# Performance work log

Measured on AMD Instinct MI355X. Metric: run time of the kernel, lower is better.

The kernel has to match this reference:

```python
import jax, jax.numpy as jnp
import numpy as np

EPS = 1e-5
THRESH = 1.5


def _compute_one(x, g_w, g_b, phi_w, phi_b, W_w, W_b, gamma, beta):
    # x: (c, w, h, z) -- single sample (torch code calls compute_x with batch 1)
    c, w, h, z = x.shape
    nz = z // 2
    # AdaptiveAvgPool3d(1) on x.permute(0,4,2,3,1): mean over (w, h, c) per z-slice -> (z,)
    p = x.mean(axis=(0, 1, 2))
    xp = x * p[None, None, None, :]
    # 1x1x1 conv projections (note: self.theta is defined but unused in the original)
    g_x = jnp.einsum('ic,cwhz->iwhz', g_w, x) + g_b[:, None, None, None]
    phi_x = jnp.einsum('ic,cwhz->iwhz', phi_w, xp) + phi_b[:, None, None, None]
    # MaxPool3d kernel (1,1,2): non-overlapping max pairs along z
    g_x = g_x.reshape(-1, w, h, nz, 2).max(axis=-1)      # (ic, w, h, nz)
    phi_x = phi_x.reshape(-1, w, h, nz, 2).max(axis=-1)  # (ic, w, h, nz)
    # theta_x: (x*p).permute(0,2,3,4,1).view(w*h, z, c)
    theta = xp.transpose(1, 2, 3, 0).reshape(w * h, z, c)
    # phi: permute(0,2,3,1,4).view(w*h, ic, nz)
    phi_m = phi_x.transpose(1, 2, 0, 3).reshape(w * h, -1, nz)
    # g: permute(0,2,3,4,1).view(w*h, nz, ic)
    g_m = g_x.transpose(1, 2, 3, 0).reshape(w * h, nz, -1)
    f = jnp.einsum('bzc,bcn->bzn', theta, phi_m)          # (wh, z, nz)
    a = jax.nn.softmax(f, axis=-1)
    y = jnp.einsum('bzn,bni->bzi', a, g_m)                # (wh, z, ic)
    y = y.reshape(w, h, z, -1).transpose(3, 0, 1, 2)      # (ic, w, h, z)
    wy = jnp.einsum('ci,iwhz->cwhz', W_w, y) + W_b[:, None, None, None]
    # BatchNorm3d in training mode on a single-sample batch: per-channel stats over (w,h,z)
    mu = wy.mean(axis=(1, 2, 3), keepdims=True)
    var = wy.var(axis=(1, 2, 3), keepdims=True)
    wy = (wy - mu) * jax.lax.rsqrt(var + EPS)
    wy = wy * gamma[:, None, None, None] + beta[:, None, None, None]
    return wy + x


def setup_inputs() -> dict:
    key = jax.random.key(0)
    ks = jax.random.split(key, 10)
    b, c, w, h, z = 2, 64, 64, 64, 64
    ic = c  # inter_channels defaults to in_channels
    x = jax.random.normal(ks[0], (b, c, w, h, z), dtype=jnp.float32)
    # spacings in [0, 3): some samples fall above spacing_thresh=1.5 (identity branch)
    spacings = jax.random.uniform(ks[1], (b, 3), dtype=jnp.float32) * 3.0
    g_w = jax.random.normal(ks[2], (ic, c), dtype=jnp.float32) * 0.1
    g_b = jax.random.normal(ks[3], (ic,), dtype=jnp.float32) * 0.1
    phi_w = jax.random.normal(ks[4], (ic, c), dtype=jnp.float32) * 0.1
    phi_b = jax.random.normal(ks[5], (ic,), dtype=jnp.float32) * 0.1
    W_w = jax.random.normal(ks[6], (c, ic), dtype=jnp.float32) * 0.1
    W_b = jax.random.normal(ks[7], (c,), dtype=jnp.float32) * 0.1
    gamma = jax.random.normal(ks[8], (c,), dtype=jnp.float32) * 0.1
    beta = jax.random.normal(ks[9], (c,), dtype=jnp.float32) * 0.1
    return {"x": x, "spacings": spacings, "g_w": g_w, "g_b": g_b,
            "phi_w": phi_w, "phi_b": phi_b, "W_w": W_w, "W_b": W_b,
            "gamma": gamma, "beta": beta}


def reference(x, spacings, g_w, g_b, phi_w, phi_b, W_w, W_b, gamma, beta):
    out = jax.vmap(_compute_one, in_axes=(0,) + (None,) * 8)(
        x, g_w, g_b, phi_w, phi_b, W_w, W_b, gamma, beta)
    use = (spacings[:, -1] <= THRESH)[:, None, None, None, None]
    return jnp.where(use, out, x)
```

## Files before the change

### kernel.cpp

```cpp
#include <hip/hip_runtime.h>
#include <hip/hip_bf16.h>
#include <math.h>

#define THRESH_SP 1.5f
#define WHZc   262144
#define CWHZc  16777216

#define WS_PSUM   0
#define WS_SLOT   128
#define WS_ZERO_N 8320
#define WS_W16_BYTE  65536
#define WS_WY_BYTE   131072
#define WS_W16_NEED  (WS_W16_BYTE + 3u*4096u*2u)
#define WS_WY_NEED   (WS_WY_BYTE + 2u*CWHZc*2u)

typedef __attribute__((ext_vector_type(8))) short bf16x8;
typedef __attribute__((ext_vector_type(4))) float floatx4;

#define MFMA(a, b, c) __builtin_amdgcn_mfma_f32_16x16x32_bf16((a), (b), (c), 0, 0, 0)

__device__ __forceinline__ unsigned short f2b(float f) {
    __hip_bfloat16 h = __float2bfloat16(f);
    return __builtin_bit_cast(unsigned short, h);
}
__device__ __forceinline__ float b2f(unsigned short h) {
    unsigned int u = ((unsigned int)h) << 16;
    return __builtin_bit_cast(float, u);
}
__device__ __forceinline__ bf16x8 ldfrag(const unsigned short* p, int elem_off) {
    return *(const bf16x8*)(p + elem_off);
}

__global__ __launch_bounds__(256) void k_prep(const float* __restrict__ gw,
                                              const float* __restrict__ pw,
                                              const float* __restrict__ Ww,
                                              float* __restrict__ ws,
                                              unsigned short* __restrict__ w16,
                                              int usew16) {
    const int i = blockIdx.x * 256 + threadIdx.x;
    if (i < WS_ZERO_N) ws[i] = 0.0f;
    if (usew16 && i < 4096) {
        w16[i]        = f2b(gw[i]);
        w16[4096 + i] = f2b(pw[i]);
        w16[8192 + i] = f2b(Ww[i]);
    }
}

__global__ __launch_bounds__(256) void k_pmean(const float* __restrict__ x,
                                               const float* __restrict__ sp,
                                               float* __restrict__ ws) {
    const int b = blockIdx.x >> 9;
    if (sp[b*3 + 2] > THRESH_SP) return;
    const int jb = blockIdx.x & 511;
    __shared__ float s[64];
    const int t = threadIdx.x;
    if (t < 64) s[t] = 0.0f;
    __syncthreads();
    const int idx4 = jb * 256 + t;
    const int z0 = (idx4 & 15) * 4;
    float a0 = 0.f, a1 = 0.f, a2 = 0.f, a3 = 0.f;
    const float* xb = x + (size_t)b * CWHZc;
#pragma unroll 4
    for (int it = 0; it < 32; ++it) {
        const float4 v = *(const float4*)&xb[(size_t)(idx4 + it * 131072) * 4];
        a0 += v.x; a1 += v.y; a2 += v.z; a3 += v.w;
    }
    a0 += __shfl_xor(a0, 16); a0 += __shfl_xor(a0, 32);
    a1 += __shfl_xor(a1, 16); a1 += __shfl_xor(a1, 32);
    a2 += __shfl_xor(a2, 16); a2 += __shfl_xor(a2, 32);
    a3 += __shfl_xor(a3, 16); a3 += __shfl_xor(a3, 32);
    if ((t & 63) < 16) {
        unsafeAtomicAdd(&s[z0 + 0], a0);
        unsafeAtomicAdd(&s[z0 + 1], a1);
        unsafeAtomicAdd(&s[z0 + 2], a2);
        unsafeAtomicAdd(&s[z0 + 3], a3);
    }
    __syncthreads();
    if (t < 64) unsafeAtomicAdd(&ws[WS_PSUM + b * 64 + t], s[t]);
}

#define L_WG     0
#define L_WP     9216
#define L_XA     18432
#define L_GPA    27648
#define L_PHA    32768
#define L_XB     37376
#define L_GPB    46592
#define L_PHB    51712
#define L_ATB    56320
#define L_BIAS   61440
#define L_PS     62208
#define L_TOTAL  62464

__global__ __launch_bounds__(512, 4) void k_main(
    const float* __restrict__ x, const float* __restrict__ sp,
    const float* __restrict__ gw, const float* __restrict__ gb,
    const float* __restrict__ pw, const float* __restrict__ pb,
    const float* __restrict__ Wwp, const float* __restrict__ Wbp,
    float* __restrict__ out, unsigned short* __restrict__ wy16, int use16,
    const unsigned short* __restrict__ w16, int usew16,
    float* __restrict__ ws) {
    const int blk = blockIdx.x;
    const int b = blk >> 11;
    if (sp[b*3 + 2] > THRESH_SP) return;
    const int whpair = (blk & 2047) * 2;

    __shared__ char smem[L_TOTAL];
    unsigned short* wg   = (unsigned short*)(smem + L_WG);
    unsigned short* wp   = (unsigned short*)(smem + L_WP);
    float*          bias = (float*)(smem + L_BIAS);
    float*          p_s  = (float*)(smem + L_PS);
    float*          statsf = (float*)(smem + L_PHA);

    const int t   = threadIdx.x;
    const int wv  = t >> 6;
    const int cid = wv >> 2;
    const int tt  = t & 255;
    const int l   = t & 63;
    const int lr  = l & 15;
    const int lq  = l >> 4;
    const int zt  = (wv & 3) << 4;

    unsigned short* xT   = (unsigned short*)(smem + (cid ? L_XB  : L_XA));
    unsigned short* gpT  = (unsigned short*)(smem + (cid ? L_GPB : L_GPA));
    unsigned short* phpN = (unsigned short*)(smem + (cid ? L_PHB : L_PHA));
    unsigned short* aT   = (unsigned short*)(smem + (cid ? L_ATB : L_WG));

    const int wh    = whpair + cid;
    const int xbase = b * CWHZc + wh * 64;

#pragma unroll
    for (int k = 0; k < 4; ++k) {
        const int f = tt + (k << 8);
        const int c = f & 63, zq = f >> 6;
        const float4 v = *(const float4*)&x[xbase + c * WHZc + zq * 4];
        xT[(zq*4 + 0)*72 + c] = f2b(v.x);
        xT[(zq*4 + 1)*72 + c] = f2b(v.y);
        xT[(zq*4 + 2)*72 + c] = f2b(v.z);
        xT[(zq*4 + 3)*72 + c] = f2b(v.w);
    }
    if (usew16) {
#pragma unroll
        for (int k = 0; k < 2; ++k) {
            const int f = t + (k << 9);
            const int mat = f >> 9;
            const int i = (f & 511) >> 3, seg = f & 7;
            unsigned short* dst = mat ? wp : wg;
            *(uint4*)&dst[i*72 + seg*8] = *(const uint4*)&w16[mat*4096 + i*64 + seg*8];
        }
    } else {
#pragma unroll
        for (int k = 0; k < 4; ++k) {
            const int f = t + (k << 9);
            const int mat = f >> 10, ff = f & 1023;
            const int i = ff >> 4, c4 = ff & 15;
            const float* src = mat ? pw : gw;
            unsigned short* dst = mat ? wp : wg;
            const float4 v = *(const float4*)&src[i*64 + c4*4];
            uint2 pk;
            pk.x = (unsigned)f2b(v.x) | ((unsigned)f2b(v.y) << 16);
            pk.y = (unsigned)f2b(v.z) | ((unsigned)f2b(v.w) << 16);
            *(uint2*)&dst[i*72 + c4*4] = pk;
        }
    }
    if (t < 192) bias[t] = (t < 64) ? gb[t] : (t < 128) ? pb[t - 64] : Wbp[t - 128];
    if (t < 64)  p_s[t] = ws[WS_PSUM + b*64 + t] * (1.0f / 262144.0f);
    __syncthreads();

    const bf16x8 a0 = ldfrag(xT, (zt + lr)*72 + lq*8);
    const bf16x8 a1 = ldfrag(xT, (zt + lr)*72 + lq*8 + 32);
    const float pz0 = p_s[zt + lq*4 + 0], pz1 = p_s[zt + lq*4 + 1];
    const float pz2 = p_s[zt + lq*4 + 2], pz3 = p_s[zt + lq*4 + 3];

    {
        const int n0 = (zt >> 1) + lq*2;
#pragma unroll
        for (int ti = 0; ti < 4; ++ti) {
            const int i = ti*16 + lr;
            const float bv = bias[i];
            floatx4 acc = {bv, bv, bv, bv};
            acc = MFMA(a0, ldfrag(wg, i*72 + lq*8), acc);
            acc = MFMA(a1, ldfrag(wg, i*72 + lq*8 + 32), acc);
            unsigned int pk = (unsigned)f2b(fmaxf(acc[0], acc[1])) |
                              ((unsigned)f2b(fmaxf(acc[2], acc[3])) << 16);
            *(unsigned int*)&gpT[i*40 + n0] = pk;
        }
    }
    __syncthreads();

    {
        const int n0 = (zt >> 1) + lq*2;
#pragma unroll
        for (int ti = 0; ti < 4; ++ti) {
            const int i = ti*16 + lr;
            floatx4 acc = {0.f, 0.f, 0.f, 0.f};
            acc = MFMA(a0, ldfrag(wp, i*72 + lq*8), acc);
            acc = MFMA(a1, ldfrag(wp, i*72 + lq*8 + 32), acc);
            const float bv = bias[64 + i];
            const float v0 = fmaf(acc[0], pz0, bv), v1 = fmaf(acc[1], pz1, bv);
            const float v2 = fmaf(acc[2], pz2, bv), v3 = fmaf(acc[3], pz3, bv);
            phpN[n0*72 + i]       = f2b(fmaxf(v0, v1));
            phpN[(n0 + 1)*72 + i] = f2b(fmaxf(v2, v3));
        }
    }
    __syncthreads();

    {
        floatx4 f0 = {0.f, 0.f, 0.f, 0.f}, f1 = {0.f, 0.f, 0.f, 0.f};
        f0 = MFMA(a0, ldfrag(phpN, lr*72 + lq*8), f0);
        f0 = MFMA(a1, ldfrag(phpN, lr*72 + lq*8 + 32), f0);
        f1 = MFMA(a0, ldfrag(phpN, (16 + lr)*72 + lq*8), f1);
        f1 = MFMA(a1, ldfrag(phpN, (16 + lr)*72 + lq*8 + 32), f1);
        if (usew16) {
            const int i = t >> 3, seg = t & 7;
            *(uint4*)&wp[i*72 + seg*8] = *(const uint4*)&w16[8192 + i*64 + seg*8];
        } else {
#pragma unroll
            for (int k = 0; k < 2; ++k) {
                const int f = t + (k << 9);
                const int i = f >> 4, c4 = f & 15;
                const float4 v = *(const float4*)&Wwp[i*64 + c4*4];
                uint2 pk;
                pk.x = (unsigned)f2b(v.x) | ((unsigned)f2b(v.y) << 16);
                pk.y = (unsigned)f2b(v.z) | ((unsigned)f2b(v.w) << 16);
                *(uint2*)&wp[i*72 + c4*4] = pk;
            }
        }
        const float pz[4] = {pz0, pz1, pz2, pz3};
#pragma unroll
        for (int r = 0; r < 4; ++r) {
            const float fr0 = f0[r] * pz[r], fr1 = f1[r] * pz[r];
            float m = fmaxf(fr0, fr1);
            m = fmaxf(m, __shfl_xor(m, 1)); m = fmaxf(m, __shfl_xor(m, 2));
            m = fmaxf(m, __shfl_xor(m, 4)); m = fmaxf(m, __shfl_xor(m, 8));
            const float e0 = __expf(fr0 - m), e1 = __expf(fr1 - m);
            float s = e0 + e1;
            s += __shfl_xor(s, 1); s += __shfl_xor(s, 2);
            s += __shfl_xor(s, 4); s += __shfl_xor(s, 8);
            const float inv = 1.0f / s;
            const int z = zt + lq*4 + r;
            aT[z*40 + lr]      = f2b(e0 * inv);
            aT[z*40 + lr + 16] = f2b(e1 * inv);
        }
    }
    __syncthreads();

    {
        if (t < 128) statsf[t] = 0.0f;
        const bf16x8 av = ldfrag(aT, (zt + lr)*40 + lq*8);
#pragma unroll
        for (int ti = 0; ti < 4; ++ti) {
            floatx4 acc = {0.f, 0.f, 0.f, 0.f};
            acc = MFMA(av, ldfrag(gpT, (ti*16 + lr)*40 + lq*8), acc);
#pragma unroll
            for (int r = 0; r < 4; ++r)
                xT[(zt + lq*4 + r)*72 + ti*16 + lr] = f2b(acc[r]);
        }
    }
    __syncthreads();

    {
        const bf16x8 y0 = ldfrag(xT, (zt + lr)*72 + lq*8);
        const bf16x8 y1 = ldfrag(xT, (zt + lr)*72 + lq*8 + 32);
#pragma unroll
        for (int ti = 0; ti < 4; ++ti) {
            const int co = ti*16 + lr;
            const float bv = bias[128 + co];
            floatx4 acc = {bv, bv, bv, bv};
            acc = MFMA(y0, ldfrag(wp, co*72 + lq*8), acc);
            acc = MFMA(y1, ldfrag(wp, co*72 + lq*8 + 32), acc);
            if (use16) {
                uint2 pk;
                pk.x = (unsigned)f2b(acc[0]) | ((unsigned)f2b(acc[1]) << 16);
                pk.y = (unsigned)f2b(acc[2]) | ((unsigned)f2b(acc[3]) << 16);
                *(uint2*)&wy16[(size_t)xbase + co * WHZc + zt + lq*4] = pk;
            } else {
                *(float4*)&out[xbase + co * WHZc + zt + lq*4] = *(float4*)&acc;
            }
            float s1 = acc[0] + acc[1] + acc[2] + acc[3];
            float s2 = acc[0]*acc[0] + acc[1]*acc[1] + acc[2]*acc[2] + acc[3]*acc[3];
            s1 += __shfl_xor(s1, 16); s1 += __shfl_xor(s1, 32);
            s2 += __shfl_xor(s2, 16); s2 += __shfl_xor(s2, 32);
            if (lq == 0) {
                atomicAdd(&statsf[co*2],     s1);
                atomicAdd(&statsf[co*2 + 1], s2);
            }
        }
    }
    __syncthreads();
    if (t < 128) {
        const int slot = blk & 31;
        unsafeAtomicAdd(&ws[WS_SLOT + (slot*2 + b)*128 + t], statsf[t]);
    }
}

__global__ __launch_bounds__(256) void k_final(const float* __restrict__ x,
                                               const float* __restrict__ sp,
                                               const float* __restrict__ gamma,
                                               const float* __restrict__ beta,
                                               float* __restrict__ out,
                                               const unsigned short* __restrict__ wy16,
                                               int use16,
                                               const float* __restrict__ ws) {
    const bool use0 = sp[2] <= THRESH_SP;
    const bool use1 = sp[5] <= THRESH_SP;
    __shared__ float scf[128], shf[128];
    if ((use0 || use1) && threadIdx.x < 128) {
        const int t = threadIdx.x;
        const int b = t >> 6, c = t & 63;
        float S1 = 0.f, S2 = 0.f;
        for (int s = 0; s < 32; s++) {
            S1 += ws[WS_SLOT + (s*2 + b)*128 + c*2 + 0];
            S2 += ws[WS_SLOT + (s*2 + b)*128 + c*2 + 1];
        }
        const float N = 262144.0f;
        const float mu = S1 / N;
        const float var = fmaxf(S2 / N - mu * mu, 0.0f);
        const float sc = gamma[c] * rsqrtf(var + 1e-5f);
        scf[t] = sc;
        shf[t] = beta[c] - mu * sc;
    }
    __syncthreads();
    const int nf4 = (2 * CWHZc) / 4;
    for (int i4 = blockIdx.x * blockDim.x + threadIdx.x; i4 < nf4;
         i4 += gridDim.x * blockDim.x) {
        const int idx = i4 * 4;
        const int b = idx >> 24;
        const bool use = b ? use1 : use0;
        const float4 xv = *(const float4*)&x[idx];
        float4 ov;
        if (use) {
            const int c = (idx >> 18) & 63;
            const float scv = scf[b * 64 + c];
            const float shv = shf[b * 64 + c];
            float w0, w1, w2, w3;
            if (use16) {
                const uint2 q = *(const uint2*)&wy16[idx];
                w0 = b2f((unsigned short)(q.x & 0xffffu));
                w1 = b2f((unsigned short)(q.x >> 16));
                w2 = b2f((unsigned short)(q.y & 0xffffu));
                w3 = b2f((unsigned short)(q.y >> 16));
            } else {
                const float4 wy = *(const float4*)&out[idx];
                w0 = wy.x; w1 = wy.y; w2 = wy.z; w3 = wy.w;
            }
            ov.x = w0 * scv + shv + xv.x;
            ov.y = w1 * scv + shv + xv.y;
            ov.z = w2 * scv + shv + xv.z;
            ov.w = w3 * scv + shv + xv.w;
        } else {
            ov = xv;
        }
        *(float4*)&out[idx] = ov;
    }
}

extern "C" void kernel_launch(void* const* d_in, const int* in_sizes, int n_in,
                              void* d_out, int out_size, void* d_ws, size_t ws_size,
                              hipStream_t stream) {
    const float* x     = (const float*)d_in[0];
    const float* spv   = (const float*)d_in[1];
    const float* gw    = (const float*)d_in[2];
    const float* gb    = (const float*)d_in[3];
    const float* pw    = (const float*)d_in[4];
    const float* pb    = (const float*)d_in[5];
    const float* Ww    = (const float*)d_in[6];
    const float* Wb    = (const float*)d_in[7];
    const float* gamma = (const float*)d_in[8];
    const float* beta  = (const float*)d_in[9];
    float* out = (float*)d_out;
    float* ws  = (float*)d_ws;
    const int usew16 = (ws_size >= (size_t)WS_W16_NEED) ? 1 : 0;
    const int use16  = (ws_size >= (size_t)WS_WY_NEED) ? 1 : 0;
    unsigned short* w16  = (unsigned short*)((char*)d_ws + WS_W16_BYTE);
    unsigned short* wy16 = (unsigned short*)((char*)d_ws + WS_WY_BYTE);

    k_prep<<<48, 256, 0, stream>>>(gw, pw, Ww, ws, w16, usew16);
    k_pmean<<<1024, 256, 0, stream>>>(x, spv, ws);
    k_main<<<4096, 512, 0, stream>>>(x, spv, gw, gb, pw, pb, Ww, Wb,
                                     out, wy16, use16, w16, usew16, ws);
    k_final<<<2048, 256, 0, stream>>>(x, spv, gamma, beta, out, wy16, use16, ws);
}
```

Measured before the change: 130.6 us.

## Swizzle LDS xT layout, reorder y MFMA for packed stores, add nontemporal epilogue

The x tile is now loaded as channel pairs and written to LDS as packed 32-bit words in an XOR-swizzled chunk layout. Fragment reads use the matching swizzle, which is meant to cut bank conflicts and the number of scalar 16-bit LDS writes. The y=a·g MFMA swaps its operands so each lane holds four consecutive channels and can write them as one 64-bit packed store. The final elementwise pass uses nontemporal loads and stores to avoid polluting the cache with streaming data.

```diff
diff --git a/kernel.cpp b/kernel.cpp
--- a/kernel.cpp
+++ b/kernel.cpp
@@ -16,6 +16,8 @@
 
 typedef __attribute__((ext_vector_type(8))) short bf16x8;
 typedef __attribute__((ext_vector_type(4))) float floatx4;
+typedef __attribute__((ext_vector_type(4))) float f32x4;
+typedef __attribute__((ext_vector_type(2))) unsigned int u32x2;
 
 #define MFMA(a, b, c) __builtin_amdgcn_mfma_f32_16x16x32_bf16((a), (b), (c), 0, 0, 0)
 
@@ -129,15 +131,31 @@
     const int wh    = whpair + cid;
     const int xbase = b * CWHZc + wh * 64;
 
-#pragma unroll
-    for (int k = 0; k < 4; ++k) {
-        const int f = tt + (k << 8);
-        const int c = f & 63, zq = f >> 6;
-        const float4 v = *(const float4*)&x[xbase + c * WHZc + zq * 4];
-        xT[(zq*4 + 0)*72 + c] = f2b(v.x);
-        xT[(zq*4 + 1)*72 + c] = f2b(v.y);
-        xT[(zq*4 + 2)*72 + c] = f2b(v.z);
-        xT[(zq*4 + 3)*72 + c] = f2b(v.w);
+    {
+        const int pr = tt >> 3;
+        const int zo = tt & 7;
+        const int c0 = pr * 2;
+        const float* xc = &x[xbase + c0 * WHZc];
+        const float4 A0 = *(const float4*)&xc[zo * 4];
+        const float4 A1 = *(const float4*)&xc[zo * 4 + 32];
+        const float4 B0 = *(const float4*)&xc[WHZc + zo * 4];
+        const float4 B1 = *(const float4*)&xc[WHZc + zo * 4 + 32];
+#pragma unroll
+        for (int g = 0; g < 2; ++g) {
+            const float4 va = g ? A1 : A0;
+            const float4 vb = g ? B1 : B0;
+            const int zb = (zo + 8 * g) * 4;
+            const float av[4] = {va.x, va.y, va.z, va.w};
+            const float bw[4] = {vb.x, vb.y, vb.z, vb.w};
+#pragma unroll
+            for (int j = 0; j < 4; ++j) {
+                const int z = zb + j;
+                const int chunk = (c0 >> 3) ^ ((z >> 2) & 3);
+                const unsigned int pk =
+                    (unsigned)f2b(av[j]) | ((unsigned)f2b(bw[j]) << 16);
+                *(unsigned int*)&xT[z * 72 + chunk * 8 + (c0 & 7)] = pk;
+            }
+        }
     }
     if (usew16) {
 #pragma unroll
@@ -167,8 +185,10 @@
     if (t < 64)  p_s[t] = ws[WS_PSUM + b*64 + t] * (1.0f / 262144.0f);
     __syncthreads();
 
-    const bf16x8 a0 = ldfrag(xT, (zt + lr)*72 + lq*8);
-    const bf16x8 a1 = ldfrag(xT, (zt + lr)*72 + lq*8 + 32);
+    const int zrow  = zt + lr;
+    const int abase = zrow * 72 + ((lq ^ ((zrow >> 2) & 3)) << 3);
+    const bf16x8 a0 = ldfrag(xT, abase);
+    const bf16x8 a1 = ldfrag(xT, abase + 32);
     const float pz0 = p_s[zt + lq*4 + 0], pz1 = p_s[zt + lq*4 + 1];
     const float pz2 = p_s[zt + lq*4 + 2], pz3 = p_s[zt + lq*4 + 3];
 
@@ -247,21 +267,27 @@
 
     {
         if (t < 128) statsf[t] = 0.0f;
-        const bf16x8 av = ldfrag(aT, (zt + lr)*40 + lq*8);
-#pragma unroll
-        for (int ti = 0; ti < 4; ++ti) {
+        const bf16x8 bv = ldfrag(aT, (zt + lr)*40 + lq*8);
+        const int zcol = zt + lr;
+        const int xzc = (zcol >> 2) & 3;
+#pragma unroll
+        for (int it = 0; it < 4; ++it) {
+            const bf16x8 av = ldfrag(gpT, (it*16 + lr)*40 + lq*8);
             floatx4 acc = {0.f, 0.f, 0.f, 0.f};
-            acc = MFMA(av, ldfrag(gpT, (ti*16 + lr)*40 + lq*8), acc);
-#pragma unroll
-            for (int r = 0; r < 4; ++r)
-                xT[(zt + lq*4 + r)*72 + ti*16 + lr] = f2b(acc[r]);
-        }
-    }
-    __syncthreads();
-
-    {
-        const bf16x8 y0 = ldfrag(xT, (zt + lr)*72 + lq*8);
-        const bf16x8 y1 = ldfrag(xT, (zt + lr)*72 + lq*8 + 32);
+            acc = MFMA(av, bv, acc);
+            const int i0 = it*16 + lq*4;
+            const int chunk = (i0 >> 3) ^ xzc;
+            uint2 pk;
+            pk.x = (unsigned)f2b(acc[0]) | ((unsigned)f2b(acc[1]) << 16);
+            pk.y = (unsigned)f2b(acc[2]) | ((unsigned)f2b(acc[3]) << 16);
+            *(uint2*)&xT[zcol*72 + chunk*8 + (i0 & 7)] = pk;
+        }
+    }
+    __syncthreads();
+
+    {
+        const bf16x8 y0 = ldfrag(xT, abase);
+        const bf16x8 y1 = ldfrag(xT, abase + 32);
 #pragma unroll
         for (int ti = 0; ti < 4; ++ti) {
             const int co = ti*16 + lr;
@@ -327,15 +353,15 @@
         const int idx = i4 * 4;
         const int b = idx >> 24;
         const bool use = b ? use1 : use0;
-        const float4 xv = *(const float4*)&x[idx];
-        float4 ov;
+        const f32x4 xv = __builtin_nontemporal_load((const f32x4*)&x[idx]);
+        f32x4 ov;
         if (use) {
             const int c = (idx >> 18) & 63;
             const float scv = scf[b * 64 + c];
             const float shv = shf[b * 64 + c];
             float w0, w1, w2, w3;
             if (use16) {
-                const uint2 q = *(const uint2*)&wy16[idx];
+                const u32x2 q = __builtin_nontemporal_load((const u32x2*)&wy16[idx]);
                 w0 = b2f((unsigned short)(q.x & 0xffffu));
                 w1 = b2f((unsigned short)(q.x >> 16));
                 w2 = b2f((unsigned short)(q.y & 0xffffu));
@@ -351,7 +377,7 @@
         } else {
             ov = xv;
         }
-        *(float4*)&out[idx] = ov;
+        __builtin_nontemporal_store(ov, (f32x4*)&out[idx]);
     }
 }
 
```

Measured after the change: 129.3 us (median of 2 runs). About the same (-1.0%).
